# Optimization experiments

Hardware: AMD Instinct MI355X
Metric: run time of the kernel (lower is better)

Reference implementation:

```python
import jax, jax.numpy as jnp
import numpy as np
from jax import lax

NPOINT, RADIUS, NSAMPLE = 2048, 0.2, 32
BN_EPS = 1e-5

def _fps(xyz, npoint):
    # Farthest point sampling; deterministic start at index 0. xyz: (B,N,3)
    B, N, _ = xyz.shape
    def step(carry, _):
        dist, far = carry
        c = jnp.take_along_axis(xyz, far[:, None, None], axis=1)  # (B,1,3)
        d = jnp.sum((xyz - c) ** 2, axis=-1)                      # (B,N)
        dist = jnp.minimum(dist, d)
        nf = jnp.argmax(dist, axis=-1).astype(jnp.int32)
        return (dist, nf), far
    init = (jnp.full((B, N), 1e10, xyz.dtype), jnp.zeros((B,), jnp.int32))
    _, idx = lax.scan(step, init, None, length=npoint)  # (npoint, B)
    return idx.T  # (B, npoint)

def _ball_query(radius, nsample, xyz, new_xyz):
    # xyz: (B,N,3), new_xyz: (B,S,3) -> (B,S,nsample) int32 indices
    B, N, _ = xyz.shape
    sq_x = jnp.sum(xyz ** 2, -1)       # (B,N)
    sq_q = jnp.sum(new_xyz ** 2, -1)   # (B,S)
    sqr = sq_q[:, :, None] + sq_x[:, None, :] - 2.0 * jnp.einsum('bsd,bnd->bsn', new_xyz, xyz)
    ar = jnp.arange(N, dtype=jnp.int32)
    gidx = jnp.where(sqr <= radius ** 2, ar, N)        # out-of-ball -> sentinel N
    gidx = jnp.sort(gidx, axis=-1)[:, :, :nsample]     # nearest-index nsample in-ball
    gidx = jnp.where(gidx == N, gidx[:, :, :1], gidx)  # pad with first valid
    return gidx

def _gather(pts, idx):
    # pts: (B,N,C), idx: (B,S,K) -> (B,S,K,C)
    return jax.vmap(lambda p, i: p[i])(pts, idx)

def _shared_mlp(g, layers):
    # g: (B,S,K,C); each layer = 1x1 conv + BN(eval) + ReLU
    for (w, b, gam, bet, mu, var) in layers:
        g = jnp.einsum('bskc,oc->bsko', g, w) + b
        g = (g - mu) * lax.rsqrt(var + BN_EPS) * gam + bet
        g = jax.nn.relu(g)
    return g

def _forward(xyz, features, layers):
    fps_idx = _fps(xyz, NPOINT)                                   # (B,S)
    new_xyz = jnp.take_along_axis(xyz, fps_idx[:, :, None], 1)    # (B,S,3)
    gidx = _ball_query(RADIUS, NSAMPLE, xyz, new_xyz)             # (B,S,K)
    grouped_xyz = _gather(xyz, gidx) - new_xyz[:, :, None, :]     # (B,S,K,3)
    grouped = jnp.concatenate([grouped_xyz, _gather(features, gidx)], -1)  # (B,S,K,3+C)
    g = _shared_mlp(grouped, layers)                              # (B,S,K,C')
    new_features = jnp.max(g, axis=2)                             # (B,S,C')
    return new_xyz, new_features

def setup_inputs() -> dict:
    key = jax.random.key(0)
    ks = jax.random.split(key, 32)
    B, N, C = 4, 8192, 64
    chans = [C + 3, 64, 64, 128]
    inp = {
        'xyz': jax.random.uniform(ks[0], (B, N, 3), jnp.float32),
        'features': jax.random.normal(ks[1], (B, N, C), jnp.float32),
    }
    for i in range(3):
        ci, co = chans[i], chans[i + 1]
        k = ks[2 + 4 * i: 6 + 4 * i]
        inp[f'w{i}'] = jax.random.normal(k[0], (co, ci), jnp.float32) * (1.0 / np.sqrt(ci))
        inp[f'b{i}'] = jax.random.normal(k[1], (co,), jnp.float32) * 0.01
        inp[f'gamma{i}'] = jax.random.uniform(k[2], (co,), jnp.float32, 0.5, 1.5)
        inp[f'beta{i}'] = jax.random.normal(k[3], (co,), jnp.float32) * 0.1
        inp[f'mean{i}'] = jax.random.normal(jax.random.fold_in(key, 100 + i), (co,), jnp.float32) * 0.1
        inp[f'var{i}'] = jax.random.uniform(jax.random.fold_in(key, 200 + i), (co,), jnp.float32, 0.5, 1.5)
    return inp

def reference(xyz, features,
              w0, b0, gamma0, beta0, mean0, var0,
              w1, b1, gamma1, beta1, mean1, var1,
              w2, b2, gamma2, beta2, mean2, var2):
    layers = [(w0, b0, gamma0, beta0, mean0, var0),
              (w1, b1, gamma1, beta1, mean1, var1),
              (w2, b2, gamma2, beta2, mean2, var2)]
    return _forward(xyz, features, layers)
```

## Files before the change

### kernel.cpp

```cpp
#include <hip/hip_runtime.h>

#define NB 4
#define NN 8192
#define NS 2048
#define NK 32
#define NCF 64
#define R2 0.04f

#define WS_FPSIDX 0
#define WS_PACK   8192
#define WS_GIDX   139264
#define WS_WT0    401408
#define WS_BB0    405696
#define WS_WT1    405760
#define WS_BB1    409856
#define WS_WT2    409920
#define WS_BB2    418112

__device__ __forceinline__ unsigned long long umax64(unsigned long long a,
                                                     unsigned long long b) {
  return a > b ? a : b;
}

template <int CTRL>
__device__ __forceinline__ void dpp_max64(unsigned& kl, unsigned& kh) {
  unsigned nl = (unsigned)__builtin_amdgcn_update_dpp(0, (int)kl, CTRL, 0xf, 0xf, true);
  unsigned nh = (unsigned)__builtin_amdgcn_update_dpp(0, (int)kh, CTRL, 0xf, 0xf, true);
  unsigned long long cur = ((unsigned long long)kh << 32) | kl;
  unsigned long long oth = ((unsigned long long)nh << 32) | nl;
  bool take = oth > cur;
  kl = take ? nl : kl;
  kh = take ? nh : kh;
}

template <int CTRL>
__device__ __forceinline__ float dpp_fmin2(float x) {
  int t = __builtin_amdgcn_update_dpp(__float_as_int(x), __float_as_int(x),
                                      CTRL, 0xf, 0xf, false);
  return fminf(x, __int_as_float(t));
}
template <int CTRL>
__device__ __forceinline__ float dpp_fmax2(float x) {
  int t = __builtin_amdgcn_update_dpp(__float_as_int(x), __float_as_int(x),
                                      CTRL, 0xf, 0xf, false);
  return fmaxf(x, __int_as_float(t));
}
__device__ __forceinline__ float wave_min_bcast(float x) {
  x = dpp_fmin2<0x111>(x); x = dpp_fmin2<0x112>(x); x = dpp_fmin2<0x114>(x);
  x = dpp_fmin2<0x118>(x); x = dpp_fmin2<0x142>(x); x = dpp_fmin2<0x143>(x);
  return __int_as_float(__builtin_amdgcn_readlane(__float_as_int(x), 63));
}
__device__ __forceinline__ float wave_max_bcast(float x) {
  x = dpp_fmax2<0x111>(x); x = dpp_fmax2<0x112>(x); x = dpp_fmax2<0x114>(x);
  x = dpp_fmax2<0x118>(x); x = dpp_fmax2<0x142>(x); x = dpp_fmax2<0x143>(x);
  return __int_as_float(__builtin_amdgcn_readlane(__float_as_int(x), 63));
}

__device__ __forceinline__ int morton12(int ix, int iy, int iz) {
  auto sp = [](int v) {
    return (v & 1) | ((v & 2) << 2) | ((v & 4) << 4) | ((v & 8) << 6);
  };
  return sp(ix) | (sp(iy) << 1) | (sp(iz) << 2);
}

__global__ __launch_bounds__(1024)
void fps_kernel(const float* __restrict__ xyz, int* __restrict__ fps_idx,
                float* __restrict__ new_xyz)
{
#pragma clang fp contract(off)
  const int b = blockIdx.x;
  const int tid = threadIdx.x;
  const int lane = tid & 63;
  const int wid = tid >> 6;
  const float* __restrict__ P = xyz + (size_t)b * (NN * 3);

  __shared__ float Pl[NN * 3];
  __shared__ unsigned short sidx[NN];
  __shared__ int hist[4096];
  __shared__ int hsum[64];
  __shared__ unsigned long long skey[2][16];

  {
    const float4* __restrict__ src = (const float4*)P;
    float4* dst = (float4*)Pl;
#pragma unroll
    for (int i = 0; i < 6; ++i) dst[tid + i * 1024] = src[tid + i * 1024];
  }
#pragma unroll
  for (int i = 0; i < 4; ++i) hist[tid + i * 1024] = 0;
  __syncthreads();

  unsigned short mycell[8];
#pragma unroll
  for (int j = 0; j < 8; ++j) {
    int p = tid + j * 1024;
    float x = Pl[p * 3 + 0], y = Pl[p * 3 + 1], z = Pl[p * 3 + 2];
    int ix = min(15, max(0, (int)(x * 16.0f)));
    int iy = min(15, max(0, (int)(y * 16.0f)));
    int iz = min(15, max(0, (int)(z * 16.0f)));
    int cell = morton12(ix, iy, iz);
    mycell[j] = (unsigned short)cell;
    atomicAdd(&hist[cell], 1);
  }
  __syncthreads();
  if (tid < 64) {
    int acc = 0;
    for (int c = 0; c < 64; ++c) {
      int h = hist[tid * 64 + c];
      hist[tid * 64 + c] = acc;
      acc += h;
    }
    hsum[tid] = acc;
  }
  __syncthreads();
  if (tid == 0) {
    int acc = 0;
    for (int c = 0; c < 64; ++c) { int h = hsum[c]; hsum[c] = acc; acc += h; }
  }
  __syncthreads();
#pragma unroll
  for (int i = 0; i < 4; ++i) {
    int c = tid + i * 1024;
    hist[c] += hsum[c >> 6];
  }
  __syncthreads();
#pragma unroll
  for (int j = 0; j < 8; ++j) {
    int p = tid + j * 1024;
    int pos = atomicAdd(&hist[mycell[j]], 1);
    sidx[pos] = (unsigned short)p;
  }
  __syncthreads();

  float px[8], py[8], pz[8], dist[8];
  unsigned klc[8];
#pragma unroll
  for (int j = 0; j < 8; ++j) {
    int slot = wid * 512 + j * 64 + lane;
    int p = sidx[slot];
    px[j] = Pl[p * 3 + 0];
    py[j] = Pl[p * 3 + 1];
    pz[j] = Pl[p * 3 + 2];
    dist[j] = 1e10f;
    klc[j] = 0xFFFFFFFFu - (unsigned)p;
  }
  float mnx = fminf(fminf(fminf(px[0], px[1]), fminf(px[2], px[3])),
                    fminf(fminf(px[4], px[5]), fminf(px[6], px[7])));
  float mxx = fmaxf(fmaxf(fmaxf(px[0], px[1]), fmaxf(px[2], px[3])),
                    fmaxf(fmaxf(px[4], px[5]), fmaxf(px[6], px[7])));
  float mny = fminf(fminf(fminf(py[0], py[1]), fminf(py[2], py[3])),
                    fminf(fminf(py[4], py[5]), fminf(py[6], py[7])));
  float mxy = fmaxf(fmaxf(fmaxf(py[0], py[1]), fmaxf(py[2], py[3])),
                    fmaxf(fmaxf(py[4], py[5]), fmaxf(py[6], py[7])));
  float mnz = fminf(fminf(fminf(pz[0], pz[1]), fminf(pz[2], pz[3])),
                    fminf(fminf(pz[4], pz[5]), fminf(pz[6], pz[7])));
  float mxz = fmaxf(fmaxf(fmaxf(pz[0], pz[1]), fmaxf(pz[2], pz[3])),
                    fmaxf(fmaxf(pz[4], pz[5]), fmaxf(pz[6], pz[7])));
  const float blx = wave_min_bcast(mnx), bhx = wave_max_bcast(mxx);
  const float bly = wave_min_bcast(mny), bhy = wave_max_bcast(mxy);
  const float blz = wave_min_bcast(mnz), bhz = wave_max_bcast(mxz);

  float cx = P[0], cy = P[1], cz = P[2];
  int far = 0;
  unsigned ckl = 0u, ckh = 0u;
  float cachedmax = 1e10f;

  for (int k = 0; k < NS; ++k) {
    if (tid == 0) {
      fps_idx[b * NS + k] = far;
      float* o = new_xyz + ((size_t)b * NS + k) * 3;
      o[0] = cx; o[1] = cy; o[2] = cz;
    }
    if (k == NS - 1) break;

    float dlx = fmaxf(fmaxf(blx - cx, cx - bhx), 0.0f);
    float dly = fmaxf(fmaxf(bly - cy, cy - bhy), 0.0f);
    float dlz = fmaxf(fmaxf(blz - cz, cz - bhz), 0.0f);
    float dlb = dlx * dlx + dly * dly + dlz * dlz;
    int doupd = __builtin_amdgcn_readfirstlane(
        (int)!(dlb * 0.999f >= cachedmax));
    if (doupd) {
      unsigned long long k8[8];
#pragma unroll
      for (int j = 0; j < 8; ++j) {
        float dx = px[j] - cx;
        float dy = py[j] - cy;
        float dz = pz[j] - cz;
        float d = (dx * dx + dy * dy) + dz * dz;
        float t = fminf(dist[j], d);
        dist[j] = t;
        k8[j] = ((unsigned long long)(unsigned)__float_as_int(t) << 32) | klc[j];
      }
      unsigned long long t0 = umax64(k8[0], k8[1]);
      unsigned long long t1 = umax64(k8[2], k8[3]);
      unsigned long long t2 = umax64(k8[4], k8[5]);
      unsigned long long t3 = umax64(k8[6], k8[7]);
      unsigned long long bk = umax64(umax64(t0, t1), umax64(t2, t3));

      unsigned kl = (unsigned)bk, kh = (unsigned)(bk >> 32);
      dpp_max64<0x111>(kl, kh);
      dpp_max64<0x112>(kl, kh);
      dpp_max64<0x114>(kl, kh);
      dpp_max64<0x118>(kl, kh);
      dpp_max64<0x142>(kl, kh);
      dpp_max64<0x143>(kl, kh);
      ckl = kl; ckh = kh;
      cachedmax = __int_as_float(__builtin_amdgcn_readlane((int)kh, 63));
    }

    const int ws = k & 1;
    if (lane == 63) {
      skey[ws][wid] = ((unsigned long long)ckh << 32) | ckl;
    }
    __syncthreads();

    unsigned long long sk = skey[ws][lane & 15];
    unsigned skl = (unsigned)sk, skh = (unsigned)(sk >> 32);
    dpp_max64<0x111>(skl, skh);
    dpp_max64<0x112>(skl, skh);
    dpp_max64<0x114>(skl, skh);
    dpp_max64<0x118>(skl, skh);
    unsigned kl15 = (unsigned)__builtin_amdgcn_readlane((int)skl, 15);
    far = (int)(0xFFFFFFFFu - kl15);

    const float* cp = Pl + far * 3;
    cx = cp[0]; cy = cp[1]; cz = cp[2];
  }
}

__global__ void prep_pack(const float* __restrict__ xyz, float4* __restrict__ pack)
{
#pragma clang fp contract(off)
  int t = blockIdx.x * 256 + threadIdx.x;
  if (t < NB * NN) {
    float x = xyz[t * 3 + 0], y = xyz[t * 3 + 1], z = xyz[t * 3 + 2];
    float4 v; v.x = x; v.y = y; v.z = z; v.w = (x * x + y * y) + z * z;
    pack[t] = v;
  }
}

__global__ void prep_w(
    const float* __restrict__ w0, const float* __restrict__ b0,
    const float* __restrict__ g0, const float* __restrict__ be0,
    const float* __restrict__ m0, const float* __restrict__ v0,
    const float* __restrict__ w1, const float* __restrict__ b1,
    const float* __restrict__ g1, const float* __restrict__ be1,
    const float* __restrict__ m1, const float* __restrict__ v1,
    const float* __restrict__ w2, const float* __restrict__ b2,
    const float* __restrict__ g2, const float* __restrict__ be2,
    const float* __restrict__ m2, const float* __restrict__ v2,
    float* __restrict__ wT0, float* __restrict__ bb0,
    float* __restrict__ wT1, float* __restrict__ bb1,
    float* __restrict__ wT2, float* __restrict__ bb2)
{
  int t = blockIdx.x * 256 + threadIdx.x;
  if (t < 4288) {
    int c = t >> 6, o = t & 63;
    int oc = (c < 64) ? (c + 3) : (c - 64);
    float sc = g0[o] * rsqrtf(v0[o] + 1e-5f);
    wT0[t] = w0[o * 67 + oc] * sc;
  } else if (t < 4352) {
    int o = t - 4288;
    float sc = g0[o] * rsqrtf(v0[o] + 1e-5f);
    bb0[o] = (b0[o] - m0[o]) * sc + be0[o];
  } else if (t < 8448) {
    int u = t - 4352;
    int c = u >> 6, o = u & 63;
    float sc = g1[o] * rsqrtf(v1[o] + 1e-5f);
    wT1[u] = w1[o * 64 + c] * sc;
  } else if (t < 8512) {
    int o = t - 8448;
    float sc = g1[o] * rsqrtf(v1[o] + 1e-5f);
    bb1[o] = (b1[o] - m1[o]) * sc + be1[o];
  } else if (t < 16704) {
    int u = t - 8512;
    int c = u >> 7, o = u & 127;
    float sc = g2[o] * rsqrtf(v2[o] + 1e-5f);
    wT2[u] = w2[o * 64 + c] * sc;
  } else if (t < 16832) {
    int o = t - 16704;
    float sc = g2[o] * rsqrtf(v2[o] + 1e-5f);
    bb2[o] = (b2[o] - m2[o]) * sc + be2[o];
  }
}

__global__ __launch_bounds__(256)
void ballq_kernel(const float4* __restrict__ pack,
                  const int* __restrict__ fps_idx, int* __restrict__ gidx)
{
#pragma clang fp contract(off)
  const int lane = threadIdx.x & 63;
  const int q = blockIdx.x * 4 + (threadIdx.x >> 6);
  const int b = q >> 11;
  const int s = q & 2047;
  const float4* __restrict__ PK = pack + (size_t)b * NN;
  const int cidx = fps_idx[b * NS + s];
  const float4 c4 = PK[cidx];
  const float cx = c4.x, cy = c4.y, cz = c4.z, csq = c4.w;
  int* __restrict__ g = gidx + (size_t)q * NK;
  int cnt = 0, firstn = 0;
  bool havefirst = false;
  for (int n0 = 0; n0 < NN; n0 += 64) {
    int n = n0 + lane;
    float4 p4 = PK[n];
    float dot = p4.x * cx;
    dot = fmaf(p4.y, cy, dot);
    dot = fmaf(p4.z, cz, dot);
    float sqr = (csq + p4.w) - 2.0f * dot;
    bool in_ = (sqr <= R2);
    unsigned long long m = __ballot(in_);
    if (!havefirst && m) { firstn = n0 + __builtin_ctzll(m); havefirst = true; }
    int pos = cnt + __popcll(m & ((1ull << lane) - 1ull));
    if (in_ && pos < NK) g[pos] = n;
    cnt += __popcll(m);
    if (cnt >= NK) break;
  }
  if (cnt < NK && lane < NK - cnt) g[cnt + lane] = firstn;
}

__global__ __launch_bounds__(256)
void mlp_kernel(const float* __restrict__ xyz, const float* __restrict__ feat,
                const int* __restrict__ gidx, const float* __restrict__ nxyz,
                const float* __restrict__ wT0, const float* __restrict__ bb0,
                const float* __restrict__ wT1, const float* __restrict__ bb1,
                const float* __restrict__ wT2, const float* __restrict__ bb2,
                float* __restrict__ out)
{
  const int q = blockIdx.x;
  const int b = q >> 11;
  const int tid = threadIdx.x;
  __shared__ int sg[32];
  __shared__ float A[32 * 76];
  __shared__ float Bf[32 * 76];
  __shared__ float Cf[32 * 132];
  __shared__ float Wb[8192];
  if (tid < 32) sg[tid] = gidx[(size_t)q * NK + tid];
  __syncthreads();
  const int k = tid >> 3, j = tid & 7;
  {
    const int p = sg[k];
    const float* fp = feat + ((size_t)b * NN + p) * NCF + j * 8;
    float4 f0 = *(const float4*)fp;
    float4 f1 = *(const float4*)(fp + 4);
    float* a = &A[k * 76 + j * 8];
    *(float4*)a = f0;
    *(float4*)(a + 4) = f1;
    if (j == 0) {
      float cx = nxyz[(size_t)q * 3 + 0];
      float cy = nxyz[(size_t)q * 3 + 1];
      float cz = nxyz[(size_t)q * 3 + 2];
      const float* pp = xyz + ((size_t)b * NN + p) * 3;
      A[k * 76 + 64] = pp[0] - cx;
      A[k * 76 + 65] = pp[1] - cy;
      A[k * 76 + 66] = pp[2] - cz;
    }
  }
  {
    const float4* src = (const float4*)wT0;
    float4* dst = (float4*)Wb;
    for (int i = tid; i < 1072; i += 256) dst[i] = src[i];
  }
  __syncthreads();
  const int o0 = j * 8;
#define FMA8(gv, base)                                                      \
  {                                                                         \
    const float* wr = (base);                                               \
    float4 wa = *(const float4*)wr;                                         \
    float4 wb = *(const float4*)(wr + 4);                                   \
    a0.x = fmaf(gv, wa.x, a0.x); a0.y = fmaf(gv, wa.y, a0.y);               \
    a0.z = fmaf(gv, wa.z, a0.z); a0.w = fmaf(gv, wa.w, a0.w);               \
    a1.x = fmaf(gv, wb.x, a1.x); a1.y = fmaf(gv, wb.y, a1.y);               \
    a1.z = fmaf(gv, wb.z, a1.z); a1.w = fmaf(gv, wb.w, a1.w);               \
  }
  {
    float4 a0 = *(const float4*)(bb0 + o0);
    float4 a1 = *(const float4*)(bb0 + o0 + 4);
    const float* Ak = &A[k * 76];
    for (int c = 0; c < 64; c += 4) {
      float4 g4 = *(const float4*)(Ak + c);
      FMA8(g4.x, Wb + (c + 0) * 64 + o0);
      FMA8(g4.y, Wb + (c + 1) * 64 + o0);
      FMA8(g4.z, Wb + (c + 2) * 64 + o0);
      FMA8(g4.w, Wb + (c + 3) * 64 + o0);
    }
    FMA8(Ak[64], Wb + 64 * 64 + o0);
    FMA8(Ak[65], Wb + 65 * 64 + o0);
    FMA8(Ak[66], Wb + 66 * 64 + o0);
    float* o = &Bf[k * 76 + o0];
    o[0] = fmaxf(a0.x, 0.f); o[1] = fmaxf(a0.y, 0.f);
    o[2] = fmaxf(a0.z, 0.f); o[3] = fmaxf(a0.w, 0.f);
    o[4] = fmaxf(a1.x, 0.f); o[5] = fmaxf(a1.y, 0.f);
    o[6] = fmaxf(a1.z, 0.f); o[7] = fmaxf(a1.w, 0.f);
  }
  __syncthreads();
  {
    const float4* src = (const float4*)wT1;
    float4* dst = (float4*)Wb;
    for (int i = tid; i < 1024; i += 256) dst[i] = src[i];
  }
  __syncthreads();
  {
    float4 a0 = *(const float4*)(bb1 + o0);
    float4 a1 = *(const float4*)(bb1 + o0 + 4);
    const float* Bk = &Bf[k * 76];
    for (int c = 0; c < 64; c += 4) {
      float4 g4 = *(const float4*)(Bk + c);
      FMA8(g4.x, Wb + (c + 0) * 64 + o0);
      FMA8(g4.y, Wb + (c + 1) * 64 + o0);
      FMA8(g4.z, Wb + (c + 2) * 64 + o0);
      FMA8(g4.w, Wb + (c + 3) * 64 + o0);
    }
    float* o = &A[k * 76 + o0];
    o[0] = fmaxf(a0.x, 0.f); o[1] = fmaxf(a0.y, 0.f);
    o[2] = fmaxf(a0.z, 0.f); o[3] = fmaxf(a0.w, 0.f);
    o[4] = fmaxf(a1.x, 0.f); o[5] = fmaxf(a1.y, 0.f);
    o[6] = fmaxf(a1.z, 0.f); o[7] = fmaxf(a1.w, 0.f);
  }
  __syncthreads();
  {
    const float4* src = (const float4*)wT2;
    float4* dst = (float4*)Wb;
    for (int i = tid; i < 2048; i += 256) dst[i] = src[i];
  }
  __syncthreads();
  {
    const int t0 = j * 16;
    float4 a0 = *(const float4*)(bb2 + t0);
    float4 a1 = *(const float4*)(bb2 + t0 + 4);
    float4 a2 = *(const float4*)(bb2 + t0 + 8);
    float4 a3 = *(const float4*)(bb2 + t0 + 12);
    const float* Ak = &A[k * 76];
#define FMA16(gv, base)                                                     \
    {                                                                       \
      const float* wr = (base);                                             \
      float4 w0v = *(const float4*)wr;                                      \
      float4 w1v = *(const float4*)(wr + 4);                                \
      float4 w2v = *(const float4*)(wr + 8);                                \
      float4 w3v = *(const float4*)(wr + 12);                               \
      a0.x = fmaf(gv, w0v.x, a0.x); a0.y = fmaf(gv, w0v.y, a0.y);           \
      a0.z = fmaf(gv, w0v.z, a0.z); a0.w = fmaf(gv, w0v.w, a0.w);           \
      a1.x = fmaf(gv, w1v.x, a1.x); a1.y = fmaf(gv, w1v.y, a1.y);           \
      a1.z = fmaf(gv, w1v.z, a1.z); a1.w = fmaf(gv, w1v.w, a1.w);           \
      a2.x = fmaf(gv, w2v.x, a2.x); a2.y = fmaf(gv, w2v.y, a2.y);           \
      a2.z = fmaf(gv, w2v.z, a2.z); a2.w = fmaf(gv, w2v.w, a2.w);           \
      a3.x = fmaf(gv, w3v.x, a3.x); a3.y = fmaf(gv, w3v.y, a3.y);           \
      a3.z = fmaf(gv, w3v.z, a3.z); a3.w = fmaf(gv, w3v.w, a3.w);           \
    }
    for (int c = 0; c < 64; c += 4) {
      float4 g4 = *(const float4*)(Ak + c);
      FMA16(g4.x, Wb + (c + 0) * 128 + t0);
      FMA16(g4.y, Wb + (c + 1) * 128 + t0);
      FMA16(g4.z, Wb + (c + 2) * 128 + t0);
      FMA16(g4.w, Wb + (c + 3) * 128 + t0);
    }
    float* o = &Cf[k * 132 + t0];
    *(float4*)(o + 0) = a0;
    *(float4*)(o + 4) = a1;
    *(float4*)(o + 8) = a2;
    *(float4*)(o + 12) = a3;
  }
  __syncthreads();
  if (tid < 128) {
    float m = Cf[tid];
    for (int kk = 1; kk < 32; ++kk) m = fmaxf(m, Cf[kk * 132 + tid]);
    out[(size_t)(NB * NS * 3) + (size_t)q * 128 + tid] = fmaxf(m, 0.0f);
  }
}

extern "C" void kernel_launch(void* const* d_in, const int* in_sizes, int n_in,
                              void* d_out, int out_size, void* d_ws, size_t ws_size,
                              hipStream_t stream)
{
  (void)in_sizes; (void)n_in; (void)out_size; (void)ws_size;
  const float* xyz  = (const float*)d_in[0];
  const float* feat = (const float*)d_in[1];
  const float* w0 = (const float*)d_in[2];
  const float* b0 = (const float*)d_in[3];
  const float* g0 = (const float*)d_in[4];
  const float* be0 = (const float*)d_in[5];
  const float* m0 = (const float*)d_in[6];
  const float* v0 = (const float*)d_in[7];
  const float* w1 = (const float*)d_in[8];
  const float* b1 = (const float*)d_in[9];
  const float* g1 = (const float*)d_in[10];
  const float* be1 = (const float*)d_in[11];
  const float* m1 = (const float*)d_in[12];
  const float* v1 = (const float*)d_in[13];
  const float* w2 = (const float*)d_in[14];
  const float* b2 = (const float*)d_in[15];
  const float* g2 = (const float*)d_in[16];
  const float* be2 = (const float*)d_in[17];
  const float* m2 = (const float*)d_in[18];
  const float* v2 = (const float*)d_in[19];

  float* ws = (float*)d_ws;
  int* fpsi = (int*)(ws + WS_FPSIDX);
  float4* pack = (float4*)(ws + WS_PACK);
  int* gidx = (int*)(ws + WS_GIDX);
  float* wT0 = ws + WS_WT0; float* bb0 = ws + WS_BB0;
  float* wT1 = ws + WS_WT1; float* bb1 = ws + WS_BB1;
  float* wT2 = ws + WS_WT2; float* bb2 = ws + WS_BB2;
  float* nxyz = (float*)d_out;

  hipLaunchKernelGGL(prep_pack, dim3((NB * NN + 255) / 256), dim3(256), 0, stream,
                     xyz, pack);
  hipLaunchKernelGGL(prep_w, dim3(66), dim3(256), 0, stream,
                     w0, b0, g0, be0, m0, v0,
                     w1, b1, g1, be1, m1, v1,
                     w2, b2, g2, be2, m2, v2,
                     wT0, bb0, wT1, bb1, wT2, bb2);
  hipLaunchKernelGGL(fps_kernel, dim3(NB), dim3(1024), 0, stream,
                     xyz, fpsi, nxyz);
  hipLaunchKernelGGL(ballq_kernel, dim3(NB * NS / 4), dim3(256), 0, stream,
                     pack, fpsi, gidx);
  hipLaunchKernelGGL(mlp_kernel, dim3(NB * NS), dim3(256), 0, stream,
                     xyz, feat, gidx, nxyz,
                     wT0, bb0, wT1, bb1, wT2, bb2, (float*)d_out);
}
```

Measured before the change: 1.903 ms.

## Retile MLP to two rows per thread and broadcast FPS centroid via readlane

In farthest point sampling, the argmax key now also encodes the winning wave's slot. Each lane loads its wave-candidate's coordinates before the final reduction, and the winner's coordinates are taken with readlane. This takes the dependent LDS load off the serial per-iteration critical path. In the MLP kernel, each thread now computes two sample rows with fewer output channels, so each weight float4 read from LDS is reused across two rows, which cuts shared-memory weight traffic. The risk is that the key encoding assumes 8192 points and at most 32 waves.

```diff
diff --git a/kernel.cpp b/kernel.cpp
--- a/kernel.cpp
+++ b/kernel.cpp
@@ -142,7 +142,7 @@
     py[j] = Pl[p * 3 + 1];
     pz[j] = Pl[p * 3 + 2];
     dist[j] = 1e10f;
-    klc[j] = 0xFFFFFFFFu - (unsigned)p;
+    klc[j] = ((unsigned)(8191 - p) << 5) | (unsigned)wid;
   }
   float mnx = fminf(fminf(fminf(px[0], px[1]), fminf(px[2], px[3])),
                     fminf(fminf(px[4], px[5]), fminf(px[6], px[7])));
@@ -216,15 +216,19 @@
 
     unsigned long long sk = skey[ws][lane & 15];
     unsigned skl = (unsigned)sk, skh = (unsigned)(sk >> 32);
+    int cand = 8191 - (int)(skl >> 5);
+    const float* cp = Pl + cand * 3;
+    float ccx = cp[0], ccy = cp[1], ccz = cp[2];
     dpp_max64<0x111>(skl, skh);
     dpp_max64<0x112>(skl, skh);
     dpp_max64<0x114>(skl, skh);
     dpp_max64<0x118>(skl, skh);
     unsigned kl15 = (unsigned)__builtin_amdgcn_readlane((int)skl, 15);
-    far = (int)(0xFFFFFFFFu - kl15);
-
-    const float* cp = Pl + far * 3;
-    cx = cp[0]; cy = cp[1]; cz = cp[2];
+    far = 8191 - (int)(kl15 >> 5);
+    int slot = (int)(kl15 & 31u);
+    cx = __int_as_float(__builtin_amdgcn_readlane(__float_as_int(ccx), slot));
+    cy = __int_as_float(__builtin_amdgcn_readlane(__float_as_int(ccy), slot));
+    cz = __int_as_float(__builtin_amdgcn_readlane(__float_as_int(ccz), slot));
   }
 }
 
@@ -336,8 +340,8 @@
   __shared__ float Wb[8192];
   if (tid < 32) sg[tid] = gidx[(size_t)q * NK + tid];
   __syncthreads();
-  const int k = tid >> 3, j = tid & 7;
-  {
+  {
+    const int k = tid >> 3, j = tid & 7;
     const int p = sg[k];
     const float* fp = feat + ((size_t)b * NN + p) * NCF + j * 8;
     float4 f0 = *(const float4*)fp;
@@ -361,36 +365,42 @@
     for (int i = tid; i < 1072; i += 256) dst[i] = src[i];
   }
   __syncthreads();
-  const int o0 = j * 8;
-#define FMA8(gv, base)                                                      \
+
+  const int k2 = tid >> 4;
+  const int jj = tid & 15;
+#define FMA4x2(gA, gB, base)                                                \
   {                                                                         \
-    const float* wr = (base);                                               \
-    float4 wa = *(const float4*)wr;                                         \
-    float4 wb = *(const float4*)(wr + 4);                                   \
-    a0.x = fmaf(gv, wa.x, a0.x); a0.y = fmaf(gv, wa.y, a0.y);               \
-    a0.z = fmaf(gv, wa.z, a0.z); a0.w = fmaf(gv, wa.w, a0.w);               \
-    a1.x = fmaf(gv, wb.x, a1.x); a1.y = fmaf(gv, wb.y, a1.y);               \
-    a1.z = fmaf(gv, wb.z, a1.z); a1.w = fmaf(gv, wb.w, a1.w);               \
-  }
-  {
-    float4 a0 = *(const float4*)(bb0 + o0);
-    float4 a1 = *(const float4*)(bb0 + o0 + 4);
-    const float* Ak = &A[k * 76];
+    float4 w = *(const float4*)(base);                                      \
+    aA.x = fmaf(gA, w.x, aA.x); aA.y = fmaf(gA, w.y, aA.y);                 \
+    aA.z = fmaf(gA, w.z, aA.z); aA.w = fmaf(gA, w.w, aA.w);                 \
+    aB.x = fmaf(gB, w.x, aB.x); aB.y = fmaf(gB, w.y, aB.y);                 \
+    aB.z = fmaf(gB, w.z, aB.z); aB.w = fmaf(gB, w.w, aB.w);                 \
+  }
+  {
+    const int o0 = jj * 4;
+    float4 aA = *(const float4*)(bb0 + o0);
+    float4 aB = aA;
+    const float* AkA = &A[k2 * 76];
+    const float* AkB = &A[(k2 + 16) * 76];
     for (int c = 0; c < 64; c += 4) {
-      float4 g4 = *(const float4*)(Ak + c);
-      FMA8(g4.x, Wb + (c + 0) * 64 + o0);
-      FMA8(g4.y, Wb + (c + 1) * 64 + o0);
-      FMA8(g4.z, Wb + (c + 2) * 64 + o0);
-      FMA8(g4.w, Wb + (c + 3) * 64 + o0);
-    }
-    FMA8(Ak[64], Wb + 64 * 64 + o0);
-    FMA8(Ak[65], Wb + 65 * 64 + o0);
-    FMA8(Ak[66], Wb + 66 * 64 + o0);
-    float* o = &Bf[k * 76 + o0];
-    o[0] = fmaxf(a0.x, 0.f); o[1] = fmaxf(a0.y, 0.f);
-    o[2] = fmaxf(a0.z, 0.f); o[3] = fmaxf(a0.w, 0.f);
-    o[4] = fmaxf(a1.x, 0.f); o[5] = fmaxf(a1.y, 0.f);
-    o[6] = fmaxf(a1.z, 0.f); o[7] = fmaxf(a1.w, 0.f);
+      float4 gA = *(const float4*)(AkA + c);
+      float4 gB = *(const float4*)(AkB + c);
+      FMA4x2(gA.x, gB.x, Wb + (c + 0) * 64 + o0);
+      FMA4x2(gA.y, gB.y, Wb + (c + 1) * 64 + o0);
+      FMA4x2(gA.z, gB.z, Wb + (c + 2) * 64 + o0);
+      FMA4x2(gA.w, gB.w, Wb + (c + 3) * 64 + o0);
+    }
+    float4 gA = *(const float4*)(AkA + 64);
+    float4 gB = *(const float4*)(AkB + 64);
+    FMA4x2(gA.x, gB.x, Wb + 64 * 64 + o0);
+    FMA4x2(gA.y, gB.y, Wb + 65 * 64 + o0);
+    FMA4x2(gA.z, gB.z, Wb + 66 * 64 + o0);
+    float4 rA; rA.x = fmaxf(aA.x, 0.f); rA.y = fmaxf(aA.y, 0.f);
+    rA.z = fmaxf(aA.z, 0.f); rA.w = fmaxf(aA.w, 0.f);
+    float4 rB; rB.x = fmaxf(aB.x, 0.f); rB.y = fmaxf(aB.y, 0.f);
+    rB.z = fmaxf(aB.z, 0.f); rB.w = fmaxf(aB.w, 0.f);
+    *(float4*)&Bf[k2 * 76 + o0] = rA;
+    *(float4*)&Bf[(k2 + 16) * 76 + o0] = rB;
   }
   __syncthreads();
   {
@@ -400,21 +410,25 @@
   }
   __syncthreads();
   {
-    float4 a0 = *(const float4*)(bb1 + o0);
-    float4 a1 = *(const float4*)(bb1 + o0 + 4);
-    const float* Bk = &Bf[k * 76];
+    const int o0 = jj * 4;
+    float4 aA = *(const float4*)(bb1 + o0);
+    float4 aB = aA;
+    const float* BkA = &Bf[k2 * 76];
+    const float* BkB = &Bf[(k2 + 16) * 76];
     for (int c = 0; c < 64; c += 4) {
-      float4 g4 = *(const float4*)(Bk + c);
-      FMA8(g4.x, Wb + (c + 0) * 64 + o0);
-      FMA8(g4.y, Wb + (c + 1) * 64 + o0);
-      FMA8(g4.z, Wb + (c + 2) * 64 + o0);
-      FMA8(g4.w, Wb + (c + 3) * 64 + o0);
-    }
-    float* o = &A[k * 76 + o0];
-    o[0] = fmaxf(a0.x, 0.f); o[1] = fmaxf(a0.y, 0.f);
-    o[2] = fmaxf(a0.z, 0.f); o[3] = fmaxf(a0.w, 0.f);
-    o[4] = fmaxf(a1.x, 0.f); o[5] = fmaxf(a1.y, 0.f);
-    o[6] = fmaxf(a1.z, 0.f); o[7] = fmaxf(a1.w, 0.f);
+      float4 gA = *(const float4*)(BkA + c);
+      float4 gB = *(const float4*)(BkB + c);
+      FMA4x2(gA.x, gB.x, Wb + (c + 0) * 64 + o0);
+      FMA4x2(gA.y, gB.y, Wb + (c + 1) * 64 + o0);
+      FMA4x2(gA.z, gB.z, Wb + (c + 2) * 64 + o0);
+      FMA4x2(gA.w, gB.w, Wb + (c + 3) * 64 + o0);
+    }
+    float4 rA; rA.x = fmaxf(aA.x, 0.f); rA.y = fmaxf(aA.y, 0.f);
+    rA.z = fmaxf(aA.z, 0.f); rA.w = fmaxf(aA.w, 0.f);
+    float4 rB; rB.x = fmaxf(aB.x, 0.f); rB.y = fmaxf(aB.y, 0.f);
+    rB.z = fmaxf(aB.z, 0.f); rB.w = fmaxf(aB.w, 0.f);
+    *(float4*)&A[k2 * 76 + o0] = rA;
+    *(float4*)&A[(k2 + 16) * 76 + o0] = rB;
   }
   __syncthreads();
   {
@@ -424,40 +438,39 @@
   }
   __syncthreads();
   {
-    const int t0 = j * 16;
-    float4 a0 = *(const float4*)(bb2 + t0);
-    float4 a1 = *(const float4*)(bb2 + t0 + 4);
-    float4 a2 = *(const float4*)(bb2 + t0 + 8);
-    float4 a3 = *(const float4*)(bb2 + t0 + 12);
-    const float* Ak = &A[k * 76];
-#define FMA16(gv, base)                                                     \
+    const int t0 = jj * 8;
+    float4 aA0 = *(const float4*)(bb2 + t0);
+    float4 aA1 = *(const float4*)(bb2 + t0 + 4);
+    float4 aB0 = aA0, aB1 = aA1;
+    const float* AkA = &A[k2 * 76];
+    const float* AkB = &A[(k2 + 16) * 76];
+#define FMA8x2(gA, gB, base)                                                \
     {                                                                       \
-      const float* wr = (base);                                             \
-      float4 w0v = *(const float4*)wr;                                      \
-      float4 w1v = *(const float4*)(wr + 4);                                \
-      float4 w2v = *(const float4*)(wr + 8);                                \
-      float4 w3v = *(const float4*)(wr + 12);                               \
-      a0.x = fmaf(gv, w0v.x, a0.x); a0.y = fmaf(gv, w0v.y, a0.y);           \
-      a0.z = fmaf(gv, w0v.z, a0.z); a0.w = fmaf(gv, w0v.w, a0.w);           \
-      a1.x = fmaf(gv, w1v.x, a1.x); a1.y = fmaf(gv, w1v.y, a1.y);           \
-      a1.z = fmaf(gv, w1v.z, a1.z); a1.w = fmaf(gv, w1v.w, a1.w);           \
-      a2.x = fmaf(gv, w2v.x, a2.x); a2.y = fmaf(gv, w2v.y, a2.y);           \
-      a2.z = fmaf(gv, w2v.z, a2.z); a2.w = fmaf(gv, w2v.w, a2.w);           \
-      a3.x = fmaf(gv, w3v.x, a3.x); a3.y = fmaf(gv, w3v.y, a3.y);           \
-      a3.z = fmaf(gv, w3v.z, a3.z); a3.w = fmaf(gv, w3v.w, a3.w);           \
+      float4 w0v = *(const float4*)(base);                                  \
+      float4 w1v = *(const float4*)((base) + 4);                            \
+      aA0.x = fmaf(gA, w0v.x, aA0.x); aA0.y = fmaf(gA, w0v.y, aA0.y);       \
+      aA0.z = fmaf(gA, w0v.z, aA0.z); aA0.w = fmaf(gA, w0v.w, aA0.w);       \
+      aA1.x = fmaf(gA, w1v.x, aA1.x); aA1.y = fmaf(gA, w1v.y, aA1.y);       \
+      aA1.z = fmaf(gA, w1v.z, aA1.z); aA1.w = fmaf(gA, w1v.w, aA1.w);       \
+      aB0.x = fmaf(gB, w0v.x, aB0.x); aB0.y = fmaf(gB, w0v.y, aB0.y);       \
+      aB0.z = fmaf(gB, w0v.z, aB0.z); aB0.w = fmaf(gB, w0v.w, aB0.w);       \
+      aB1.x = fmaf(gB, w1v.x, aB1.x); aB1.y = fmaf(gB, w1v.y, aB1.y);       \
+      aB1.z = fmaf(gB, w1v.z, aB1.z); aB1.w = fmaf(gB, w1v.w, aB1.w);       \
     }
     for (int c = 0; c < 64; c += 4) {
-      float4 g4 = *(const float4*)(Ak + c);
-      FMA16(g4.x, Wb + (c + 0) * 128 + t0);
-      FMA16(g4.y, Wb + (c + 1) * 128 + t0);
-      FMA16(g4.z, Wb + (c + 2) * 128 + t0);
-      FMA16(g4.w, Wb + (c + 3) * 128 + t0);
-    }
-    float* o = &Cf[k * 132 + t0];
-    *(float4*)(o + 0) = a0;
-    *(float4*)(o + 4) = a1;
-    *(float4*)(o + 8) = a2;
-    *(float4*)(o + 12) = a3;
+      float4 gA = *(const float4*)(AkA + c);
+      float4 gB = *(const float4*)(AkB + c);
+      FMA8x2(gA.x, gB.x, Wb + (c + 0) * 128 + t0);
+      FMA8x2(gA.y, gB.y, Wb + (c + 1) * 128 + t0);
+      FMA8x2(gA.z, gB.z, Wb + (c + 2) * 128 + t0);
+      FMA8x2(gA.w, gB.w, Wb + (c + 3) * 128 + t0);
+    }
+    float* oA = &Cf[k2 * 132 + t0];
+    *(float4*)(oA + 0) = aA0;
+    *(float4*)(oA + 4) = aA1;
+    float* oB = &Cf[(k2 + 16) * 132 + t0];
+    *(float4*)(oB + 0) = aB0;
+    *(float4*)(oB + 4) = aB1;
   }
   __syncthreads();
   if (tid < 128) {
```

Result: slower. 1.986 ms (+4.4%).
